# Kernel optimization log

Hardware: AMD Instinct MI355X
Metric: run time of the kernel (lower is better)

Reference implementation:

```python
import jax, jax.numpy as jnp
import numpy as np

NUM_USERS = 200000
NUM_ITEMS = 100000
DIM = 64
NUM_LAYERS = 2
NUM_EDGES = 3200000
EPS = 1e-12  # F.normalize eps


def setup_inputs() -> dict:
    key = jax.random.key(0)
    ks = jax.random.split(key, 8)
    return {
        "user_emb": jax.random.normal(ks[0], (NUM_USERS, DIM), dtype=jnp.float32),
        "item_emb": jax.random.normal(ks[1], (NUM_ITEMS, DIM), dtype=jnp.float32),
        "Wu": jax.random.normal(ks[2], (NUM_LAYERS, DIM, 2 * DIM), dtype=jnp.float32) * 0.1,
        "Wi": jax.random.normal(ks[3], (NUM_LAYERS, DIM, 2 * DIM), dtype=jnp.float32) * 0.1,
        "u_idx": jax.random.randint(ks[4], (NUM_EDGES,), 0, NUM_USERS, dtype=jnp.int32),
        "i_idx": jax.random.randint(ks[5], (NUM_EDGES,), 0, NUM_ITEMS, dtype=jnp.int32),
        "w_u2i": jax.random.uniform(ks[6], (NUM_EDGES,), dtype=jnp.float32),
        "w_i2u": jax.random.uniform(ks[7], (NUM_EDGES,), dtype=jnp.float32),
    }


def _l2_normalize(x):
    # matches F.normalize(p=2, dim=1): x / max(||x||, eps)
    n = jnp.sqrt(jnp.sum(x * x, axis=1, keepdims=True))
    return x / jnp.maximum(n, EPS)


def _spmm(vals, rows, cols, h, num_rows):
    # (sparse [num_rows, num_cols]) @ h : gather rows of h at cols, scale, scatter-add
    msg = vals[:, None] * h[cols]  # [E, DIM]
    return jax.ops.segment_sum(msg, rows, num_segments=num_rows)


def reference(user_emb, item_emb, Wu, Wi, u_idx, i_idx, w_u2i, w_i2u):
    h_u, h_i = user_emb, item_emb
    for l in range(NUM_LAYERS):
        neigh_u = _spmm(w_u2i, u_idx, i_idx, h_i, NUM_USERS)   # adj_u2i @ h_i
        neigh_i = _spmm(w_i2u, i_idx, u_idx, h_u, NUM_ITEMS)   # adj_i2u @ h_u
        # Linear(2*dim -> dim, no bias): concat then x @ W.T
        h_u_new = jax.nn.relu(jnp.concatenate([h_u, neigh_u], axis=1) @ Wu[l].T)
        h_i_new = jax.nn.relu(jnp.concatenate([h_i, neigh_i], axis=1) @ Wi[l].T)
        h_u = _l2_normalize(h_u_new)
        h_i = _l2_normalize(h_i_new)
    return (h_u, h_i)
```

## Files before the change

kernel.cpp:

```cpp
#include <hip/hip_runtime.h>


#define N_USERS 200000
#define N_ITEMS 100000
#define N_EDGES 3200000
#define NB_U 782
#define NB_I 391

typedef float v2f __attribute__((ext_vector_type(2)));

__global__ __launch_bounds__(256) void wprep_kernel(
    const float* __restrict__ Wu, const float* __restrict__ Wi,
    float* __restrict__ WuT, float* __restrict__ WiT)
{
    int idx = blockIdx.x * 256 + threadIdx.x;
    const float* src = Wu;
    float* dst = WuT;
    int i = idx;
    if (idx >= 16384) { src = Wi; dst = WiT; i = idx - 16384; }
    int l = i >> 13;
    int r = i & 8191;
    int j = r >> 7;
    int k = r & 127;
    dst[l * 8192 + k * 64 + j] = src[i];
}

__global__ __launch_bounds__(256) void hist_kernel(
    const int* __restrict__ u_idx, const int* __restrict__ i_idx,
    int* __restrict__ deg_u, int* __restrict__ deg_i,
    unsigned short* __restrict__ rank_u, unsigned short* __restrict__ rank_i)
{
    int t = blockIdx.x * 256 + threadIdx.x;
    if (t < N_EDGES) {
        rank_u[t] = (unsigned short)atomicAdd(&deg_u[u_idx[t]], 1);
    } else {
        int e = t - N_EDGES;
        rank_i[e] = (unsigned short)atomicAdd(&deg_i[i_idx[e]], 1);
    }
}

__global__ __launch_bounds__(256) void scanA_kernel(
    const int* __restrict__ deg_u, const int* __restrict__ deg_i,
    int* __restrict__ bsum_u, int* __restrict__ bsum_i)
{
    int b = blockIdx.x;
    const int* deg; int n; int* bs; int bb;
    if (b < NB_U) { deg = deg_u; n = N_USERS; bs = bsum_u; bb = b; }
    else          { deg = deg_i; n = N_ITEMS; bs = bsum_i; bb = b - NB_U; }
    int i = bb * 256 + threadIdx.x;
    int v = (i < n) ? deg[i] : 0;
    #pragma unroll
    for (int off = 1; off < 64; off <<= 1) v += __shfl_xor(v, off);
    __shared__ int ws4[4];
    int wv = threadIdx.x >> 6;
    if ((threadIdx.x & 63) == 0) ws4[wv] = v;
    __syncthreads();
    if (threadIdx.x == 0) bs[bb] = ws4[0] + ws4[1] + ws4[2] + ws4[3];
}

__global__ __launch_bounds__(1024) void scanB_kernel(
    const int* __restrict__ bsum_u, int* __restrict__ bpre_u,
    const int* __restrict__ bsum_i, int* __restrict__ bpre_i)
{
    __shared__ int s[1024];
    const int* src; int* dst; int n;
    if (blockIdx.x == 0) { src = bsum_u; dst = bpre_u; n = NB_U; }
    else                 { src = bsum_i; dst = bpre_i; n = NB_I; }
    int t = threadIdx.x;
    int v = (t < n) ? src[t] : 0;
    s[t] = v; __syncthreads();
    #pragma unroll
    for (int off = 1; off < 1024; off <<= 1) {
        int x = (t >= off) ? s[t - off] : 0;
        __syncthreads();
        s[t] += x;
        __syncthreads();
    }
    if (t < n) dst[t] = s[t] - v;
}

__global__ __launch_bounds__(256) void scanC_kernel(
    const int* __restrict__ deg_u, const int* __restrict__ deg_i,
    const int* __restrict__ bpre_u, const int* __restrict__ bpre_i,
    int* __restrict__ rowptr_u, int* __restrict__ rowptr_i)
{
    int b = blockIdx.x;
    const int* deg; int n; const int* bpre; int* rowptr; int bb;
    if (b < NB_U) { deg = deg_u; n = N_USERS; bpre = bpre_u; rowptr = rowptr_u; bb = b; }
    else          { deg = deg_i; n = N_ITEMS; bpre = bpre_i; rowptr = rowptr_i; bb = b - NB_U; }
    int t = threadIdx.x;
    int i = bb * 256 + t;
    int d = (i < n) ? deg[i] : 0;
    __shared__ int s[256];
    s[t] = d; __syncthreads();
    #pragma unroll
    for (int off = 1; off < 256; off <<= 1) {
        int x = (t >= off) ? s[t - off] : 0;
        __syncthreads();
        s[t] += x;
        __syncthreads();
    }
    int val = bpre[bb] + (s[t] - d);
    if (i < n) rowptr[i] = val;
    if (b == 0 && t == 0) { rowptr_u[N_USERS] = N_EDGES; rowptr_i[N_ITEMS] = N_EDGES; }
}

__global__ __launch_bounds__(256) void fill_kernel(
    const int* __restrict__ u_idx, const int* __restrict__ i_idx,
    const float* __restrict__ w_u2i, const float* __restrict__ w_i2u,
    const unsigned short* __restrict__ rank_u, const unsigned short* __restrict__ rank_i,
    const int* __restrict__ rowptr_u, const int* __restrict__ rowptr_i,
    uint2* __restrict__ edges_u, uint2* __restrict__ edges_i)
{
    const int part   = blockIdx.x & 7;
    const int slot   = blockIdx.x >> 3;
    const int nslots = gridDim.x >> 3;
    const int stride = nslots * 256;

    for (int e = slot * 256 + threadIdx.x; e < N_EDGES; e += stride) {
        int ru = u_idx[e];
        int ri = i_idx[e];
        if ((ru & 7) == part) {
            int p = rowptr_u[ru] + rank_u[e];
            edges_u[p] = make_uint2((unsigned)ri, __float_as_uint(w_u2i[e]));
        }
        if ((ri & 7) == part) {
            int p = rowptr_i[ri] + rank_i[e];
            edges_i[p] = make_uint2((unsigned)ru, __float_as_uint(w_i2u[e]));
        }
    }
}

#define XSW(rr) ((((rr) >> 1) & 3) << 3)

__global__ __launch_bounds__(256, 4) void transform_fused_kernel(
    const float* __restrict__ hself_u, const float* __restrict__ hsrc_u,
    const int* __restrict__ rowptr_u, const uint2* __restrict__ edges_u,
    const float* __restrict__ WtU, float* __restrict__ out_u,
    const float* __restrict__ hself_i, const float* __restrict__ hsrc_i,
    const int* __restrict__ rowptr_i, const uint2* __restrict__ edges_i,
    const float* __restrict__ WtI, float* __restrict__ out_i,
    int nbu)
{
    __shared__ float Ws[64 * 64];
    __shared__ float Xs[64 * 64];
    int* rp_s = (int*)Ws;

    const int tid = threadIdx.x;

    const int nbt = (int)gridDim.x;
    const int nbi = nbt - nbu;
    int bid = (int)blockIdx.x;
    int g = bid / 3, r = bid - 3 * g;
    bool is_u; int bb;
    if (r < 2) {
        int cand = 2 * g + r;
        if (cand < nbu) { is_u = true;  bb = cand; }
        else            { is_u = false; bb = nbi - (nbt - bid); }
    } else {
        int cand = g;
        if (cand < nbi) { is_u = false; bb = cand; }
        else            { is_u = true;  bb = nbu - (nbt - bid); }
    }

    const float* hself; const float* hsrc; const int* rowptr;
    const uint2* edges; const float* Wt; float* out; int N;
    if (is_u) {
        hself = hself_u; hsrc = hsrc_u; rowptr = rowptr_u; edges = edges_u;
        Wt = WtU; out = out_u; N = N_USERS;
    } else {
        hself = hself_i; hsrc = hsrc_i; rowptr = rowptr_i; edges = edges_i;
        Wt = WtI; out = out_i; N = N_ITEMS;
    }
    const int row0 = bb * 64;

    {
        const float4* wsrc = (const float4*)Wt;
        float4* wdst = (float4*)Ws;
        #pragma unroll
        for (int i = 0; i < 4; ++i) wdst[tid + i * 256] = wsrc[tid + i * 256];
        #pragma unroll
        for (int i = 0; i < 4; ++i) {
            int idx4 = tid + i * 256;
            int rr = idx4 >> 4, c4 = idx4 & 15;
            int gr = row0 + rr; if (gr > N - 1) gr = N - 1;
            float4 v = ((const float4*)(hself + (size_t)gr * 64))[c4];
            ((float4*)Xs)[(rr << 4) + (c4 ^ (XSW(rr) >> 2))] = v;
        }
    }
    __syncthreads();

    const int tr = tid >> 3;
    const int tc = tid & 7;
    const int r0 = 2 * tr;
    const int xsw = XSW(r0);

    v2f acc2[2][4];
    #pragma unroll
    for (int j = 0; j < 2; ++j)
        #pragma unroll
        for (int c = 0; c < 4; ++c) acc2[j][c] = (v2f){0.f, 0.f};

    #pragma unroll 8
    for (int k = 0; k < 64; ++k) {
        float a0 = Xs[(r0 << 6) + (k ^ xsw)];
        float a1 = Xs[((r0 + 1) << 6) + (k ^ xsw)];
        float4 b0 = *(const float4*)&Ws[k * 64 + 8 * tc];
        float4 b1 = *(const float4*)&Ws[k * 64 + 8 * tc + 4];
        v2f bv0 = {b0.x, b0.y}, bv1 = {b0.z, b0.w};
        v2f bv2 = {b1.x, b1.y}, bv3 = {b1.z, b1.w};
        v2f a0v = {a0, a0}, a1v = {a1, a1};
        acc2[0][0] += a0v * bv0; acc2[0][1] += a0v * bv1;
        acc2[0][2] += a0v * bv2; acc2[0][3] += a0v * bv3;
        acc2[1][0] += a1v * bv0; acc2[1][1] += a1v * bv1;
        acc2[1][2] += a1v * bv2; acc2[1][3] += a1v * bv3;
    }
    __syncthreads();

    {
        float4 z = make_float4(0.f, 0.f, 0.f, 0.f);
        #pragma unroll
        for (int i = 0; i < 4; ++i) ((float4*)Xs)[tid + i * 256] = z;
        if (tid <= 64) rp_s[tid] = rowptr[min(row0 + tid, N)];
    }
    __syncthreads();

    {
        const int wv = tid >> 6;
        const int ln = tid & 63;
        const int e0 = rp_s[0], e1 = rp_s[64];
        const int perw = (e1 - e0 + 3) >> 2;
        const int wsb  = e0 + wv * perw;
        const int web  = min(wsb + perw, e1);
        const int clen = (web - wsb + 7) >> 3;

        int   cs[8], ce[8], rr[8], nend[8];
        float gacc[8];
        uint2 ec[8];
        #pragma unroll
        for (int c = 0; c < 8; ++c) {
            cs[c] = wsb + c * clen;
            ce[c] = min(cs[c] + clen, web);
            gacc[c] = 0.f;
            int lo = 0, hi = 64;
            #pragma unroll
            for (int s = 0; s < 6; ++s) {
                int mid = (lo + hi) >> 1;
                bool go = rp_s[mid] <= cs[c];
                lo = go ? mid : lo;
                hi = go ? hi : mid;
            }
            rr[c] = lo; nend[c] = rp_s[lo + 1];
            ec[c] = edges[min(cs[c], N_EDGES - 1)];
        }

        #pragma unroll 1
        for (int it = 0; it < clen; ++it) {
            float hv[8], wg[8];
            #pragma unroll
            for (int c = 0; c < 8; ++c) {
                bool v = (cs[c] + it) < ce[c];
                wg[c] = v ? __uint_as_float(ec[c].y) : 0.f;
                hv[c] = hsrc[(int)ec[c].x * 64 + ln];
            }
            #pragma unroll
            for (int c = 0; c < 8; ++c)
                ec[c] = edges[min(cs[c] + it + 1, N_EDGES - 1)];
            #pragma unroll
            for (int c = 0; c < 8; ++c) {
                gacc[c] = fmaf(wg[c], hv[c], gacc[c]);
                int p   = cs[c] + it;
                int nxt = p + 1;
                if (p < ce[c] && (nxt == nend[c] || nxt == ce[c])) {
                    atomicAdd(&Xs[(rr[c] << 6) + (ln ^ XSW(rr[c]))], gacc[c]);
                    gacc[c] = 0.f;
                    if (nxt == nend[c] && nxt < web) {
                        int r2 = rr[c];
                        while (r2 < 63 && rp_s[r2 + 1] <= nxt) ++r2;
                        rr[c] = r2; nend[c] = rp_s[r2 + 1];
                    }
                }
            }
        }
    }
    __syncthreads();

    {
        const float4* wsrc = (const float4*)(Wt + 4096);
        float4* wdst = (float4*)Ws;
        #pragma unroll
        for (int i = 0; i < 4; ++i) wdst[tid + i * 256] = wsrc[tid + i * 256];
    }
    __syncthreads();

    #pragma unroll 8
    for (int k = 0; k < 64; ++k) {
        float a0 = Xs[(r0 << 6) + (k ^ xsw)];
        float a1 = Xs[((r0 + 1) << 6) + (k ^ xsw)];
        float4 b0 = *(const float4*)&Ws[k * 64 + 8 * tc];
        float4 b1 = *(const float4*)&Ws[k * 64 + 8 * tc + 4];
        v2f bv0 = {b0.x, b0.y}, bv1 = {b0.z, b0.w};
        v2f bv2 = {b1.x, b1.y}, bv3 = {b1.z, b1.w};
        v2f a0v = {a0, a0}, a1v = {a1, a1};
        acc2[0][0] += a0v * bv0; acc2[0][1] += a0v * bv1;
        acc2[0][2] += a0v * bv2; acc2[0][3] += a0v * bv3;
        acc2[1][0] += a1v * bv0; acc2[1][1] += a1v * bv1;
        acc2[1][2] += a1v * bv2; acc2[1][3] += a1v * bv3;
    }

    #pragma unroll
    for (int j = 0; j < 2; ++j) {
        float v[8];
        v[0] = fmaxf(acc2[j][0].x, 0.f); v[1] = fmaxf(acc2[j][0].y, 0.f);
        v[2] = fmaxf(acc2[j][1].x, 0.f); v[3] = fmaxf(acc2[j][1].y, 0.f);
        v[4] = fmaxf(acc2[j][2].x, 0.f); v[5] = fmaxf(acc2[j][2].y, 0.f);
        v[6] = fmaxf(acc2[j][3].x, 0.f); v[7] = fmaxf(acc2[j][3].y, 0.f);
        float s = 0.f;
        #pragma unroll
        for (int c = 0; c < 8; ++c) s = fmaf(v[c], v[c], s);
        s += __shfl_xor(s, 1);
        s += __shfl_xor(s, 2);
        s += __shfl_xor(s, 4);
        float nrm = sqrtf(s);
        float inv = 1.f / fmaxf(nrm, 1e-12f);
        int gr = row0 + r0 + j;
        if (gr < N) {
            float4 o0 = make_float4(v[0]*inv, v[1]*inv, v[2]*inv, v[3]*inv);
            float4 o1 = make_float4(v[4]*inv, v[5]*inv, v[6]*inv, v[7]*inv);
            float* p = out + gr * 64 + 8 * tc;
            *(float4*)p       = o0;
            *(float4*)(p + 4) = o1;
        }
    }
}

extern "C" void kernel_launch(void* const* d_in, const int* in_sizes, int n_in,
                              void* d_out, int out_size, void* d_ws, size_t ws_size,
                              hipStream_t stream)
{
    (void)in_sizes; (void)n_in; (void)out_size; (void)ws_size;

    const float* user_emb = (const float*)d_in[0];
    const float* item_emb = (const float*)d_in[1];
    const float* Wu       = (const float*)d_in[2];
    const float* Wi       = (const float*)d_in[3];
    const int*   u_idx    = (const int*)d_in[4];
    const int*   i_idx    = (const int*)d_in[5];
    const float* w_u2i    = (const float*)d_in[6];
    const float* w_i2u    = (const float*)d_in[7];
    float* out = (float*)d_out;

    float* ws      = (float*)d_ws;
    float* WuT     = ws;
    float* WiT     = WuT + 16384;
    float* hu1     = WiT + 16384;
    float* hi1     = hu1 + N_USERS * 64;
    uint2* edges_u = (uint2*)(hi1 + N_ITEMS * 64);
    uint2* edges_i = edges_u + N_EDGES;
    unsigned short* rank_u = (unsigned short*)(edges_i + N_EDGES);
    unsigned short* rank_i = rank_u + N_EDGES;
    int* rowptr_u = (int*)(rank_i + N_EDGES);
    int* rowptr_i = rowptr_u + (N_USERS + 1);
    int* deg_u    = rowptr_i + (N_ITEMS + 1);
    int* deg_i    = deg_u + N_USERS;
    int* bsum_u   = deg_i + N_ITEMS;
    int* bpre_u   = bsum_u + NB_U;
    int* bsum_i   = bpre_u + NB_U;
    int* bpre_i   = bsum_i + NB_I;

    const int tu_blocks = (N_USERS + 63) / 64;
    const int ti_blocks = (N_ITEMS + 63) / 64;
    const int e2_blocks = (2 * N_EDGES) / 256;

    wprep_kernel<<<128, 256, 0, stream>>>(Wu, Wi, WuT, WiT);
    hipMemsetAsync(deg_u, 0, (size_t)(N_USERS + N_ITEMS) * 4, stream);
    hist_kernel<<<e2_blocks, 256, 0, stream>>>(u_idx, i_idx, deg_u, deg_i, rank_u, rank_i);
    scanA_kernel<<<NB_U + NB_I, 256, 0, stream>>>(deg_u, deg_i, bsum_u, bsum_i);
    scanB_kernel<<<2, 1024, 0, stream>>>(bsum_u, bpre_u, bsum_i, bpre_i);
    scanC_kernel<<<NB_U + NB_I, 256, 0, stream>>>(deg_u, deg_i, bpre_u, bpre_i, rowptr_u, rowptr_i);
    fill_kernel<<<2048, 256, 0, stream>>>(u_idx, i_idx, w_u2i, w_i2u,
                                          rank_u, rank_i, rowptr_u, rowptr_i,
                                          edges_u, edges_i);

    transform_fused_kernel<<<tu_blocks + ti_blocks, 256, 0, stream>>>(
        user_emb, item_emb, rowptr_u, edges_u, WuT, hu1,
        item_emb, user_emb, rowptr_i, edges_i, WiT, hi1, tu_blocks);

    transform_fused_kernel<<<tu_blocks + ti_blocks, 256, 0, stream>>>(
        hu1, hi1, rowptr_u, edges_u, WuT + 8192, out,
        hi1, hu1, rowptr_i, edges_i, WiT + 8192, out + (size_t)N_USERS * 64, tu_blocks);
}
```

Baseline: 1.399 ms.

## Halve weight LDS tile and raise occupancy target of fused transform kernel

The weight staging buffer in shared memory shrinks from 64x64 to 32x64 floats. Each 64-wide matmul phase now loads two K-halves in sequence, separated by extra barriers. The launch bound rises from 4 to 6 blocks per CU, so more blocks can be resident to hide gather latency in the sparse aggregation. In exchange it adds extra barriers and weight reloads, and the tighter register budget could cause spills.

```diff
diff --git a/kernel.cpp b/kernel.cpp
--- a/kernel.cpp
+++ b/kernel.cpp
@@ -133,7 +133,7 @@
 
 #define XSW(rr) ((((rr) >> 1) & 3) << 3)
 
-__global__ __launch_bounds__(256, 4) void transform_fused_kernel(
+__global__ __launch_bounds__(256, 6) void transform_fused_kernel(
     const float* __restrict__ hself_u, const float* __restrict__ hsrc_u,
     const int* __restrict__ rowptr_u, const uint2* __restrict__ edges_u,
     const float* __restrict__ WtU, float* __restrict__ out_u,
@@ -142,7 +142,7 @@
     const float* __restrict__ WtI, float* __restrict__ out_i,
     int nbu)
 {
-    __shared__ float Ws[64 * 64];
+    __shared__ float Ws[32 * 64];
     __shared__ float Xs[64 * 64];
     int* rp_s = (int*)Ws;
 
@@ -174,11 +174,22 @@
     }
     const int row0 = bb * 64;
 
+    const int tr = tid >> 3;
+    const int tc = tid & 7;
+    const int r0 = 2 * tr;
+    const int xsw = XSW(r0);
+
+    v2f acc2[2][4];
+    #pragma unroll
+    for (int j = 0; j < 2; ++j)
+        #pragma unroll
+        for (int c = 0; c < 4; ++c) acc2[j][c] = (v2f){0.f, 0.f};
+
     {
         const float4* wsrc = (const float4*)Wt;
         float4* wdst = (float4*)Ws;
-        #pragma unroll
-        for (int i = 0; i < 4; ++i) wdst[tid + i * 256] = wsrc[tid + i * 256];
+        wdst[tid]       = wsrc[tid];
+        wdst[tid + 256] = wsrc[tid + 256];
         #pragma unroll
         for (int i = 0; i < 4; ++i) {
             int idx4 = tid + i * 256;
@@ -190,23 +201,38 @@
     }
     __syncthreads();
 
-    const int tr = tid >> 3;
-    const int tc = tid & 7;
-    const int r0 = 2 * tr;
-    const int xsw = XSW(r0);
-
-    v2f acc2[2][4];
-    #pragma unroll
-    for (int j = 0; j < 2; ++j)
-        #pragma unroll
-        for (int c = 0; c < 4; ++c) acc2[j][c] = (v2f){0.f, 0.f};
-
     #pragma unroll 8
-    for (int k = 0; k < 64; ++k) {
-        float a0 = Xs[(r0 << 6) + (k ^ xsw)];
-        float a1 = Xs[((r0 + 1) << 6) + (k ^ xsw)];
-        float4 b0 = *(const float4*)&Ws[k * 64 + 8 * tc];
-        float4 b1 = *(const float4*)&Ws[k * 64 + 8 * tc + 4];
+    for (int k2 = 0; k2 < 32; ++k2) {
+        int kk = k2;
+        float a0 = Xs[(r0 << 6) + (kk ^ xsw)];
+        float a1 = Xs[((r0 + 1) << 6) + (kk ^ xsw)];
+        float4 b0 = *(const float4*)&Ws[k2 * 64 + 8 * tc];
+        float4 b1 = *(const float4*)&Ws[k2 * 64 + 8 * tc + 4];
+        v2f bv0 = {b0.x, b0.y}, bv1 = {b0.z, b0.w};
+        v2f bv2 = {b1.x, b1.y}, bv3 = {b1.z, b1.w};
+        v2f a0v = {a0, a0}, a1v = {a1, a1};
+        acc2[0][0] += a0v * bv0; acc2[0][1] += a0v * bv1;
+        acc2[0][2] += a0v * bv2; acc2[0][3] += a0v * bv3;
+        acc2[1][0] += a1v * bv0; acc2[1][1] += a1v * bv1;
+        acc2[1][2] += a1v * bv2; acc2[1][3] += a1v * bv3;
+    }
+    __syncthreads();
+
+    {
+        const float4* wsrc = (const float4*)(Wt + 2048);
+        float4* wdst = (float4*)Ws;
+        wdst[tid]       = wsrc[tid];
+        wdst[tid + 256] = wsrc[tid + 256];
+    }
+    __syncthreads();
+
+    #pragma unroll 8
+    for (int k2 = 0; k2 < 32; ++k2) {
+        int kk = 32 + k2;
+        float a0 = Xs[(r0 << 6) + (kk ^ xsw)];
+        float a1 = Xs[((r0 + 1) << 6) + (kk ^ xsw)];
+        float4 b0 = *(const float4*)&Ws[k2 * 64 + 8 * tc];
+        float4 b1 = *(const float4*)&Ws[k2 * 64 + 8 * tc + 4];
         v2f bv0 = {b0.x, b0.y}, bv1 = {b0.z, b0.w};
         v2f bv2 = {b1.x, b1.y}, bv3 = {b1.z, b1.w};
         v2f a0v = {a0, a0}, a1v = {a1, a1};
@@ -288,17 +314,43 @@
     {
         const float4* wsrc = (const float4*)(Wt + 4096);
         float4* wdst = (float4*)Ws;
-        #pragma unroll
-        for (int i = 0; i < 4; ++i) wdst[tid + i * 256] = wsrc[tid + i * 256];
+        wdst[tid]       = wsrc[tid];
+        wdst[tid + 256] = wsrc[tid + 256];
     }
     __syncthreads();
 
     #pragma unroll 8
-    for (int k = 0; k < 64; ++k) {
-        float a0 = Xs[(r0 << 6) + (k ^ xsw)];
-        float a1 = Xs[((r0 + 1) << 6) + (k ^ xsw)];
-        float4 b0 = *(const float4*)&Ws[k * 64 + 8 * tc];
-        float4 b1 = *(const float4*)&Ws[k * 64 + 8 * tc + 4];
+    for (int k2 = 0; k2 < 32; ++k2) {
+        int kk = k2;
+        float a0 = Xs[(r0 << 6) + (kk ^ xsw)];
+        float a1 = Xs[((r0 + 1) << 6) + (kk ^ xsw)];
+        float4 b0 = *(const float4*)&Ws[k2 * 64 + 8 * tc];
+        float4 b1 = *(const float4*)&Ws[k2 * 64 + 8 * tc + 4];
+        v2f bv0 = {b0.x, b0.y}, bv1 = {b0.z, b0.w};
+        v2f bv2 = {b1.x, b1.y}, bv3 = {b1.z, b1.w};
+        v2f a0v = {a0, a0}, a1v = {a1, a1};
+        acc2[0][0] += a0v * bv0; acc2[0][1] += a0v * bv1;
+        acc2[0][2] += a0v * bv2; acc2[0][3] += a0v * bv3;
+        acc2[1][0] += a1v * bv0; acc2[1][1] += a1v * bv1;
+        acc2[1][2] += a1v * bv2; acc2[1][3] += a1v * bv3;
+    }
+    __syncthreads();
+
+    {
+        const float4* wsrc = (const float4*)(Wt + 6144);
+        float4* wdst = (float4*)Ws;
+        wdst[tid]       = wsrc[tid];
+        wdst[tid + 256] = wsrc[tid + 256];
+    }
+    __syncthreads();
+
+    #pragma unroll 8
+    for (int k2 = 0; k2 < 32; ++k2) {
+        int kk = 32 + k2;
+        float a0 = Xs[(r0 << 6) + (kk ^ xsw)];
+        float a1 = Xs[((r0 + 1) << 6) + (kk ^ xsw)];
+        float4 b0 = *(const float4*)&Ws[k2 * 64 + 8 * tc];
+        float4 b1 = *(const float4*)&Ws[k2 * 64 + 8 * tc + 4];
         v2f bv0 = {b0.x, b0.y}, bv1 = {b0.z, b0.w};
         v2f bv2 = {b1.x, b1.y}, bv3 = {b1.z, b1.w};
         v2f a0v = {a0, a0}, a1v = {a1, a1};
```

Measured after the change: 4.315 ms. +208.4%, slower.
